# Performance work log

Measured on AMD Instinct MI355X. Metric: run time of the kernel, lower is better.

Reference implementation:

```python
import math
import jax, jax.numpy as jnp
import numpy as np

D_MODEL = 2048
NUM_EXPERTS = 64
Z_LOSS_COEF = 1e-3
AUX_LOSS_COEF = 1e-2
CAPACITY_FACTOR = 1.0
MIN_CAPACITY = 4


def setup_inputs() -> dict:
    key = jax.random.key(0)
    kx, kw = jax.random.split(key)
    x = jax.random.normal(kx, (4, 4096, D_MODEL), dtype=jnp.float32)
    W = 0.02 * jax.random.normal(kw, (NUM_EXPERTS, D_MODEL), dtype=jnp.float32)  # gate weight [E, D]
    return {"x": x, "W": W}


def reference(x, W):
    B, T, D = x.shape
    N = B * T                      # num_tokens
    E = W.shape[0]
    x_flat = x.reshape(N, D)

    logits = jnp.einsum("nd,ed->ne", x_flat, W)          # gate GEMM [N, E]
    probs = jax.nn.softmax(logits, axis=-1)

    # z-loss: mean(logsumexp(logits)^2)
    z_loss = jnp.mean(jnp.square(jax.nn.logsumexp(logits, axis=-1)))

    expert_index = jnp.argmax(logits, axis=-1)            # [N] int
    expert_prob = jnp.take_along_axis(probs, expert_index[:, None], axis=-1)[:, 0]  # [N]

    counts = jnp.bincount(expert_index, length=E)         # [E] int
    f_i = counts.astype(probs.dtype) / N                  # fraction routed per expert
    p_i = jnp.mean(probs, axis=0)                         # mean router prob per expert
    aux_loss = AUX_LOSS_COEF * E * jnp.sum(f_i * p_i) + Z_LOSS_COEF * z_loss

    capacity = max(MIN_CAPACITY, math.ceil(CAPACITY_FACTOR * N / E))  # static int
    return expert_index, expert_prob, counts, capacity, aux_loss
```

## Files before the change

### kernel.cpp

```cpp
#include <hip/hip_runtime.h>
#include <math.h>

#define D_MODEL 2048
#define NE      64
#define TB      64
#define KSEG    1024
#define KC      128
#define NCH     (KSEG / KC)
#define FB_KC   32
#define FB_NCH  (D_MODEL / FB_KC)

typedef _Float16 half8 __attribute__((ext_vector_type(8)));
typedef float    f32x4 __attribute__((ext_vector_type(4)));

#define CVT1(F, HV, LV, J) do {                                               \
    float _f = (F);                                                           \
    _Float16 _h = (_Float16)_f;                                               \
    HV[J] = _h;                                                               \
    LV[J] = (_Float16)(_f - (float)_h);                                       \
} while (0)

__global__ __launch_bounds__(256) void wcvt_kernel(
    const float* __restrict__ W, short* __restrict__ Wh, short* __restrict__ Wl)
{
    const int e = blockIdx.x, t = threadIdx.x, c = t * 8;
    const float* src = W + (size_t)e * D_MODEL + c;
    float4 v0 = *(const float4*)src;
    float4 v1 = *(const float4*)(src + 4);
    half8 hv, lv;
    CVT1(v0.x * 64.0f, hv, lv, 0); CVT1(v0.y * 64.0f, hv, lv, 1);
    CVT1(v0.z * 64.0f, hv, lv, 2); CVT1(v0.w * 64.0f, hv, lv, 3);
    CVT1(v1.x * 64.0f, hv, lv, 4); CVT1(v1.y * 64.0f, hv, lv, 5);
    CVT1(v1.z * 64.0f, hv, lv, 6); CVT1(v1.w * 64.0f, hv, lv, 7);
    *(half8*)(Wh + (size_t)e * D_MODEL + c) = hv;
    *(half8*)(Wl + (size_t)e * D_MODEL + c) = lv;
}

__global__ __launch_bounds__(512) void router_fused8(
    const float* __restrict__ x, const short* __restrict__ Whg,
    const short* __restrict__ Wlg, float* __restrict__ out,
    float* __restrict__ ws_prob, float* __restrict__ ws_z,
    int* __restrict__ ws_cnt, int Ntok)
{
    __shared__ __align__(16) char smem[131072];

    const int t  = threadIdx.x;
    const int b  = blockIdx.x;
    const int m0 = b * TB;
    const int g  = t >> 8;
    const int tg = t & 255;
    const int l  = tg & 63;
    const int wv = tg >> 6;
    const int k0 = g * KSEG;

    char* gb = smem + g * 65536;
    _Float16* Ah = (_Float16*)gb;
    _Float16* Al = (_Float16*)(gb + 16384);
    _Float16* Wh = (_Float16*)(gb + 32768);
    _Float16* Wl = (_Float16*)(gb + 49152);

    float (*sL)[NE + 1] = (float (*)[NE + 1])smem;
    float (*red8)[8]    = (float (*)[8])(smem + 16640);
    int   (*arg8)[8]    = (int (*)[8])(smem + 18688);
    float* smax         = (float*)(smem + 20736);
    float* sinv         = (float*)(smem + 20992);
    float (*spart)[NE]  = (float (*)[NE])(smem + 21248);
    int*   hist         = (int*)(smem + 23296);

    const int srow  = tg >> 4;
    const int sslt  = tg & 15;
    const int soff0 = ((sslt ^ (srow & 7)) << 3);

    float4 paA0, paA1, paA2, paA3, paA4, paA5, paA6, paA7;
    float4 paB0, paB1, paB2, paB3, paB4, paB5, paB6, paB7;
    uint4  pwh0, pwh1, pwh2, pwh3, pwl0, pwl1, pwl2, pwl3;

#define PRE_A(P0, P1, P2, P3, P4, P5, P6, P7, KB) do {                        \
    const float* _a0 = x + (size_t)(m0 +  0 + srow) * D_MODEL + (KB) + sslt * 8; \
    const float* _a1 = x + (size_t)(m0 + 16 + srow) * D_MODEL + (KB) + sslt * 8; \
    const float* _a2 = x + (size_t)(m0 + 32 + srow) * D_MODEL + (KB) + sslt * 8; \
    const float* _a3 = x + (size_t)(m0 + 48 + srow) * D_MODEL + (KB) + sslt * 8; \
    P0 = *(const float4*)_a0; P1 = *(const float4*)(_a0 + 4);                 \
    P2 = *(const float4*)_a1; P3 = *(const float4*)(_a1 + 4);                 \
    P4 = *(const float4*)_a2; P5 = *(const float4*)(_a2 + 4);                 \
    P6 = *(const float4*)_a3; P7 = *(const float4*)(_a3 + 4);                 \
} while (0)

#define PRE_W(KB) do {                                                        \
    const size_t _w0 = (size_t)( 0 + srow) * D_MODEL + (KB) + sslt * 8;       \
    const size_t _w1 = (size_t)(16 + srow) * D_MODEL + (KB) + sslt * 8;       \
    const size_t _w2 = (size_t)(32 + srow) * D_MODEL + (KB) + sslt * 8;       \
    const size_t _w3 = (size_t)(48 + srow) * D_MODEL + (KB) + sslt * 8;       \
    pwh0 = *(const uint4*)&Whg[_w0]; pwh1 = *(const uint4*)&Whg[_w1];         \
    pwh2 = *(const uint4*)&Whg[_w2]; pwh3 = *(const uint4*)&Whg[_w3];         \
    pwl0 = *(const uint4*)&Wlg[_w0]; pwl1 = *(const uint4*)&Wlg[_w1];         \
    pwl2 = *(const uint4*)&Wlg[_w2]; pwl3 = *(const uint4*)&Wlg[_w3];         \
} while (0)

#define STORE_ITEM(I, PA, PB, PWH, PWL) do {                                  \
    half8 _hv, _lv;                                                           \
    CVT1((PA).x * 8.0f, _hv, _lv, 0); CVT1((PA).y * 8.0f, _hv, _lv, 1);       \
    CVT1((PA).z * 8.0f, _hv, _lv, 2); CVT1((PA).w * 8.0f, _hv, _lv, 3);       \
    CVT1((PB).x * 8.0f, _hv, _lv, 4); CVT1((PB).y * 8.0f, _hv, _lv, 5);       \
    CVT1((PB).z * 8.0f, _hv, _lv, 6); CVT1((PB).w * 8.0f, _hv, _lv, 7);       \
    const int _off = ((I) * 16 + srow) * 128 + soff0;                         \
    *(half8*)&Ah[_off] = _hv;                                                 \
    *(half8*)&Al[_off] = _lv;                                                 \
    *(uint4*)&Wh[_off] = PWH;                                                 \
    *(uint4*)&Wl[_off] = PWL;                                                 \
} while (0)

#define STORE_SET(P0, P1, P2, P3, P4, P5, P6, P7) do {                        \
    STORE_ITEM(0, P0, P1, pwh0, pwl0);                                        \
    STORE_ITEM(1, P2, P3, pwh1, pwl1);                                        \
    STORE_ITEM(2, P4, P5, pwh2, pwl2);                                        \
    STORE_ITEM(3, P6, P7, pwh3, pwl3);                                        \
} while (0)

#define MFMA_PHASE() do {                                                     \
    const int arow = wv * 16 + (l & 15);                                      \
    const int rsw  = l & 7;                                                   \
    _Pragma("unroll")                                                         \
    for (int kq = 0; kq < 4; ++kq) {                                          \
        const int s    = kq * 4 + (l >> 4);                                   \
        const int aoff = arow * 128 + ((s ^ rsw) << 3);                       \
        half8 ah = *(const half8*)&Ah[aoff];                                  \
        half8 al = *(const half8*)&Al[aoff];                                  \
        _Pragma("unroll")                                                     \
        for (int n = 0; n < 4; ++n) {                                         \
            const int woff = (n * 16 + (l & 15)) * 128 + ((s ^ rsw) << 3);    \
            half8 wh = *(const half8*)&Wh[woff];                              \
            half8 wl = *(const half8*)&Wl[woff];                              \
            f32x4 a = (n == 0) ? acc0 : (n == 1) ? acc1 : (n == 2) ? acc2 : acc3; \
            a = __builtin_amdgcn_mfma_f32_16x16x32_f16(al, wl, a, 0, 0, 0);   \
            a = __builtin_amdgcn_mfma_f32_16x16x32_f16(al, wh, a, 0, 0, 0);   \
            a = __builtin_amdgcn_mfma_f32_16x16x32_f16(ah, wl, a, 0, 0, 0);   \
            a = __builtin_amdgcn_mfma_f32_16x16x32_f16(ah, wh, a, 0, 0, 0);   \
            if (n == 0) acc0 = a; else if (n == 1) acc1 = a;                  \
            else if (n == 2) acc2 = a; else acc3 = a;                         \
        }                                                                     \
    }                                                                         \
} while (0)

    f32x4 acc0 = {0.f,0.f,0.f,0.f}, acc1 = {0.f,0.f,0.f,0.f};
    f32x4 acc2 = {0.f,0.f,0.f,0.f}, acc3 = {0.f,0.f,0.f,0.f};

    PRE_A(paA0, paA1, paA2, paA3, paA4, paA5, paA6, paA7, k0);
    PRE_W(k0);
    PRE_A(paB0, paB1, paB2, paB3, paB4, paB5, paB6, paB7, k0 + KC);

    for (int ch = 0; ch < NCH; ch += 2) {
        __builtin_amdgcn_s_barrier();
        STORE_SET(paA0, paA1, paA2, paA3, paA4, paA5, paA6, paA7);
        asm volatile("s_waitcnt lgkmcnt(0)" ::: "memory");
        __builtin_amdgcn_s_barrier();
        if (ch + 1 < NCH) PRE_W(k0 + (ch + 1) * KC);
        if (ch + 2 < NCH)
            PRE_A(paA0, paA1, paA2, paA3, paA4, paA5, paA6, paA7, k0 + (ch + 2) * KC);
        MFMA_PHASE();
        __builtin_amdgcn_s_barrier();
        STORE_SET(paB0, paB1, paB2, paB3, paB4, paB5, paB6, paB7);
        asm volatile("s_waitcnt lgkmcnt(0)" ::: "memory");
        __builtin_amdgcn_s_barrier();
        if (ch + 2 < NCH) PRE_W(k0 + (ch + 2) * KC);
        if (ch + 3 < NCH)
            PRE_A(paB0, paB1, paB2, paB3, paB4, paB5, paB6, paB7, k0 + (ch + 3) * KC);
        MFMA_PHASE();
    }

    __syncthreads();
    const int rbase = wv * 16 + (l >> 4) * 4;
    const int col0  = l & 15;
    if (g == 1) {
        #pragma unroll
        for (int q = 0; q < 4; ++q) {
            sL[rbase + q][ 0 + col0] = acc0[q];
            sL[rbase + q][16 + col0] = acc1[q];
            sL[rbase + q][32 + col0] = acc2[q];
            sL[rbase + q][48 + col0] = acc3[q];
        }
    }
    __syncthreads();
    if (g == 0) {
        #pragma unroll
        for (int q = 0; q < 4; ++q) {
            sL[rbase + q][ 0 + col0] = (acc0[q] + sL[rbase + q][ 0 + col0]) * (1.0f / 512.0f);
            sL[rbase + q][16 + col0] = (acc1[q] + sL[rbase + q][16 + col0]) * (1.0f / 512.0f);
            sL[rbase + q][32 + col0] = (acc2[q] + sL[rbase + q][32 + col0]) * (1.0f / 512.0f);
            sL[rbase + q][48 + col0] = (acc3[q] + sL[rbase + q][48 + col0]) * (1.0f / 512.0f);
        }
    }
    if (t < NE) hist[t] = 0;
    __syncthreads();

    {
        const int m = t >> 3, qr = t & 7;
        float mx = -3.4e38f; int ag = qr * 8;
        #pragma unroll
        for (int k = 0; k < 8; ++k) {
            const int e = qr * 8 + k;
            float v = sL[m][e];
            if (v > mx) { mx = v; ag = e; }
        }
        red8[m][qr] = mx; arg8[m][qr] = ag;
    }
    __syncthreads();
    if (t < 64) {
        const int m = t;
        float mx = red8[m][0]; int ag = arg8[m][0];
        #pragma unroll
        for (int qr = 1; qr < 8; ++qr)
            if (red8[m][qr] > mx) { mx = red8[m][qr]; ag = arg8[m][qr]; }
        smax[m] = mx;
        out[m0 + m] = (float)ag;
        atomicAdd(&hist[ag], 1);
    }
    __syncthreads();
    {
        const int m = t >> 3, qr = t & 7;
        const float mx = smax[m];
        float s = 0.f;
        #pragma unroll
        for (int k = 0; k < 8; ++k) s += expf(sL[m][qr * 8 + k] - mx);
        red8[m][qr] = s;
    }
    __syncthreads();
    if (t < 64) {
        const int m = t;
        float s = 0.f;
        #pragma unroll
        for (int qr = 0; qr < 8; ++qr) s += red8[m][qr];
        float inv = 1.f / s;
        sinv[m] = inv;
        out[Ntok + m0 + m] = inv;
        float lse = smax[m] + logf(s);
        float z = lse * lse;
        #pragma unroll
        for (int off = 32; off > 0; off >>= 1) z += __shfl_down(z, off, 64);
        if (t == 0) ws_z[b] = z;
    }
    __syncthreads();
    {
        const int e = t & 63, gw = t >> 6;
        float pa = 0.f;
        #pragma unroll
        for (int k = 0; k < 8; ++k) {
            const int m = gw * 8 + k;
            pa += expf(sL[m][e] - smax[m]) * sinv[m];
        }
        spart[gw][e] = pa;
    }
    __syncthreads();
    if (t < NE) {
        float ps = 0.f;
        #pragma unroll
        for (int gw = 0; gw < 8; ++gw) ps += spart[gw][t];
        ws_prob[b * NE + t] = ps;
        ws_cnt[b * NE + t]  = hist[t];
    }
}

__global__ __launch_bounds__(256) void router_final2(
    const float* __restrict__ ws_prob, const float* __restrict__ ws_z,
    const int* __restrict__ ws_cnt, float* __restrict__ out,
    int Ntok, int nblocks)
{
    __shared__ float sp[4][NE];
    __shared__ int   sc[4][NE];
    __shared__ float sz[4];

    const int e = threadIdx.x & 63, g = threadIdx.x >> 6;
    const int per = nblocks / 4;
    const int hi  = (g == 3) ? nblocks : (g + 1) * per;

    float ps = 0.f; int c = 0;
    for (int blk = g * per; blk < hi; ++blk) {
        ps += ws_prob[blk * NE + e];
        c  += ws_cnt[blk * NE + e];
    }
    sp[g][e] = ps; sc[g][e] = c;

    float z = 0.f;
    for (int blk = (int)threadIdx.x; blk < nblocks; blk += 256) z += ws_z[blk];
    #pragma unroll
    for (int off = 32; off > 0; off >>= 1) z += __shfl_down(z, off, 64);
    if (e == 0) sz[g] = z;
    __syncthreads();

    if (threadIdx.x < 64) {
        const int ee = threadIdx.x;
        float pst = ((sp[0][ee] + sp[1][ee]) + sp[2][ee]) + sp[3][ee];
        int   ct  = ((sc[0][ee] + sc[1][ee]) + sc[2][ee]) + sc[3][ee];
        out[2 * Ntok + ee] = (float)ct;

        float fN = (float)Ntok;
        float fp = ((float)ct / fN) * (pst / fN);
        #pragma unroll
        for (int off = 32; off > 0; off >>= 1) fp += __shfl_down(fp, off, 64);
        if (ee == 0) {
            float zt = ((sz[0] + sz[1]) + sz[2]) + sz[3];
            int cap = (Ntok + NE - 1) / NE;
            if (cap < 4) cap = 4;
            float aux = 0.01f * (float)NE * fp + 1e-3f * (zt / fN);
            out[2 * Ntok + NE]     = (float)cap;
            out[2 * Ntok + NE + 1] = aux;
        }
    }
}

__global__ __launch_bounds__(256) void router_main_fb(
    const float* __restrict__ x, const float* __restrict__ W,
    float* __restrict__ out, float* __restrict__ ws_prob,
    float* __restrict__ ws_z, int* __restrict__ ws_cnt, int Ntok)
{
    __shared__ __align__(16) float sX[FB_KC][68];
    __shared__ __align__(16) float sW[FB_KC][68];
    __shared__ float sL[64][65];
    __shared__ float smax[64], sinv[64];
    __shared__ float spart[4][NE];
    __shared__ int   hist[NE];

    const int t = threadIdx.x, b = blockIdx.x, m0 = b * 64;
    const int mq = t & 15, nq = t >> 4;
    const int r1 = t >> 3, r2 = r1 + 32, c1 = (t & 7) << 2;
    const float* xp1 = x + (size_t)(m0 + r1) * D_MODEL + c1;
    const float* xp2 = x + (size_t)(m0 + r2) * D_MODEL + c1;
    const float* wp1 = W + (size_t)r1 * D_MODEL + c1;
    const float* wp2 = W + (size_t)r2 * D_MODEL + c1;
    float4 ax1 = *(const float4*)xp1, ax2 = *(const float4*)xp2;
    float4 aw1 = *(const float4*)wp1, aw2 = *(const float4*)wp2;
    float a1[4][4] = {}, a2[4][4] = {};
    for (int ch = 0; ch < FB_NCH; ++ch) {
        __syncthreads();
        sX[c1+0][r1] = ax1.x; sX[c1+1][r1] = ax1.y; sX[c1+2][r1] = ax1.z; sX[c1+3][r1] = ax1.w;
        sX[c1+0][r2] = ax2.x; sX[c1+1][r2] = ax2.y; sX[c1+2][r2] = ax2.z; sX[c1+3][r2] = ax2.w;
        sW[c1+0][r1] = aw1.x; sW[c1+1][r1] = aw1.y; sW[c1+2][r1] = aw1.z; sW[c1+3][r1] = aw1.w;
        sW[c1+0][r2] = aw2.x; sW[c1+1][r2] = aw2.y; sW[c1+2][r2] = aw2.z; sW[c1+3][r2] = aw2.w;
        __syncthreads();
        if (ch + 1 < FB_NCH) {
            xp1 += FB_KC; xp2 += FB_KC; wp1 += FB_KC; wp2 += FB_KC;
            ax1 = *(const float4*)xp1; ax2 = *(const float4*)xp2;
            aw1 = *(const float4*)wp1; aw2 = *(const float4*)wp2;
        }
        #pragma unroll
        for (int k = 0; k < FB_KC; ++k) {
            float4 xa = *(const float4*)&sX[k][mq << 2];
            float4 wb = *(const float4*)&sW[k][nq << 2];
            float (*A)[4] = (k < FB_KC / 2) ? a1 : a2;
            A[0][0] = fmaf(xa.x, wb.x, A[0][0]); A[0][1] = fmaf(xa.x, wb.y, A[0][1]);
            A[0][2] = fmaf(xa.x, wb.z, A[0][2]); A[0][3] = fmaf(xa.x, wb.w, A[0][3]);
            A[1][0] = fmaf(xa.y, wb.x, A[1][0]); A[1][1] = fmaf(xa.y, wb.y, A[1][1]);
            A[1][2] = fmaf(xa.y, wb.z, A[1][2]); A[1][3] = fmaf(xa.y, wb.w, A[1][3]);
            A[2][0] = fmaf(xa.z, wb.x, A[2][0]); A[2][1] = fmaf(xa.z, wb.y, A[2][1]);
            A[2][2] = fmaf(xa.z, wb.z, A[2][2]); A[2][3] = fmaf(xa.z, wb.w, A[2][3]);
            A[3][0] = fmaf(xa.w, wb.x, A[3][0]); A[3][1] = fmaf(xa.w, wb.y, A[3][1]);
            A[3][2] = fmaf(xa.w, wb.z, A[3][2]); A[3][3] = fmaf(xa.w, wb.w, A[3][3]);
        }
    }
    #pragma unroll
    for (int i = 0; i < 4; ++i)
        #pragma unroll
        for (int j = 0; j < 4; ++j)
            sL[(mq << 2) + i][(nq << 2) + j] = a1[i][j] + a2[i][j];
    if (t < NE) hist[t] = 0;
    __syncthreads();
    if (t < 64) {
        const int m = t;
        float mx = sL[m][0]; int arg = 0;
        for (int e = 1; e < NE; ++e) { float v = sL[m][e]; if (v > mx) { mx = v; arg = e; } }
        float s = 0.f;
        for (int e = 0; e < NE; ++e) s += expf(sL[m][e] - mx);
        float inv = 1.f / s;
        out[m0 + m] = (float)arg; out[Ntok + m0 + m] = inv;
        smax[m] = mx; sinv[m] = inv;
        atomicAdd(&hist[arg], 1);
        float lse = mx + logf(s); float z = lse * lse;
        for (int off = 32; off > 0; off >>= 1) z += __shfl_down(z, off, 64);
        if (t == 0) ws_z[b] = z;
    }
    __syncthreads();
    {
        const int e = t & 63, mg = t >> 6;
        float pa = 0.f;
        for (int m = mg * 16; m < mg * 16 + 16; ++m) pa += expf(sL[m][e] - smax[m]) * sinv[m];
        spart[mg][e] = pa;
    }
    __syncthreads();
    if (t < NE) {
        ws_prob[b * NE + t] = spart[0][t] + spart[1][t] + spart[2][t] + spart[3][t];
        ws_cnt[b * NE + t]  = hist[t];
    }
}

extern "C" void kernel_launch(void* const* d_in, const int* in_sizes, int n_in,
                              void* d_out, int out_size, void* d_ws, size_t ws_size,
                              hipStream_t stream)
{
    const float* x = (const float*)d_in[0];
    const float* W = (const float*)d_in[1];
    float* out = (float*)d_out;

    const int Ntok = in_sizes[0] / D_MODEL;
    const int nblk = Ntok / TB;

    const size_t wh_elems = (size_t)NE * D_MODEL;
    const size_t need = wh_elems * 2 * 2
                      + ((size_t)nblk * NE + nblk) * 4
                      + (size_t)nblk * NE * 4 + 1024;

    if ((Ntok % TB) == 0 && (nblk % 4) == 0 && ws_size >= need) {
        short* wsh     = (short*)d_ws;
        short* wsl     = wsh + wh_elems;
        float* ws_prob = (float*)(wsl + wh_elems);
        float* ws_z    = ws_prob + (size_t)nblk * NE;
        int*   ws_cnt  = (int*)(ws_z + nblk);

        wcvt_kernel<<<NE, 256, 0, stream>>>(W, wsh, wsl);
        router_fused8<<<nblk, 512, 0, stream>>>(x, wsh, wsl, out,
                                                ws_prob, ws_z, ws_cnt, Ntok);
        router_final2<<<1, 256, 0, stream>>>(ws_prob, ws_z, ws_cnt, out, Ntok, nblk);
    } else {
        const int nb = Ntok / 64;
        float* ws_prob = (float*)d_ws;
        float* ws_z    = ws_prob + (size_t)nb * NE;
        int*   ws_cnt  = (int*)(ws_z + nb);
        router_main_fb<<<nb, 256, 0, stream>>>(x, W, out, ws_prob, ws_z, ws_cnt, Ntok);
        router_final2<<<1, 256, 0, stream>>>(ws_prob, ws_z, ws_cnt, out, Ntok, nb);
    }
}
```

Measured before the change: 61.72 us.

## Double-buffer LDS tiles with halved K chunk to overlap stores and MFMA

Halves the K chunk from 128 to 64 and splits each group's 64KB shared region into two 32KB buffers, so the next chunk's converted A and W tiles are written to one buffer while MFMAs read the other. This drops one barrier per chunk and overlaps LDS stores with matrix math. The global load pattern also changes: each thread now loads one row with contiguous 16-element segments instead of four rows of 8 elements. In exchange there are twice as many chunks, each with less MFMA work to hide latency behind, and register-held prefetch now covers both A and W for two sets.

```diff
diff --git a/kernel.cpp b/kernel.cpp
--- a/kernel.cpp
+++ b/kernel.cpp
@@ -5,7 +5,7 @@
 #define NE      64
 #define TB      64
 #define KSEG    1024
-#define KC      128
+#define KC      64
 #define NCH     (KSEG / KC)
 #define FB_KC   32
 #define FB_NCH  (D_MODEL / FB_KC)
@@ -36,7 +36,7 @@
     *(half8*)(Wl + (size_t)e * D_MODEL + c) = lv;
 }
 
-__global__ __launch_bounds__(512) void router_fused8(
+__global__ __launch_bounds__(512) void router_fused_db(
     const float* __restrict__ x, const short* __restrict__ Whg,
     const short* __restrict__ Wlg, float* __restrict__ out,
     float* __restrict__ ws_prob, float* __restrict__ ws_z,
@@ -53,11 +53,7 @@
     const int wv = tg >> 6;
     const int k0 = g * KSEG;
 
-    char* gb = smem + g * 65536;
-    _Float16* Ah = (_Float16*)gb;
-    _Float16* Al = (_Float16*)(gb + 16384);
-    _Float16* Wh = (_Float16*)(gb + 32768);
-    _Float16* Wl = (_Float16*)(gb + 49152);
+    char* gbase = smem + g * 65536;
 
     float (*sL)[NE + 1] = (float (*)[NE + 1])smem;
     float (*red8)[8]    = (float (*)[8])(smem + 16640);
@@ -67,70 +63,64 @@
     float (*spart)[NE]  = (float (*)[NE])(smem + 21248);
     int*   hist         = (int*)(smem + 23296);
 
-    const int srow  = tg >> 4;
-    const int sslt  = tg & 15;
-    const int soff0 = ((sslt ^ (srow & 7)) << 3);
-
-    float4 paA0, paA1, paA2, paA3, paA4, paA5, paA6, paA7;
-    float4 paB0, paB1, paB2, paB3, paB4, paB5, paB6, paB7;
-    uint4  pwh0, pwh1, pwh2, pwh3, pwl0, pwl1, pwl2, pwl3;
-
-#define PRE_A(P0, P1, P2, P3, P4, P5, P6, P7, KB) do {                        \
-    const float* _a0 = x + (size_t)(m0 +  0 + srow) * D_MODEL + (KB) + sslt * 8; \
-    const float* _a1 = x + (size_t)(m0 + 16 + srow) * D_MODEL + (KB) + sslt * 8; \
-    const float* _a2 = x + (size_t)(m0 + 32 + srow) * D_MODEL + (KB) + sslt * 8; \
-    const float* _a3 = x + (size_t)(m0 + 48 + srow) * D_MODEL + (KB) + sslt * 8; \
-    P0 = *(const float4*)_a0; P1 = *(const float4*)(_a0 + 4);                 \
-    P2 = *(const float4*)_a1; P3 = *(const float4*)(_a1 + 4);                 \
-    P4 = *(const float4*)_a2; P5 = *(const float4*)(_a2 + 4);                 \
-    P6 = *(const float4*)_a3; P7 = *(const float4*)(_a3 + 4);                 \
+    const int srow = tg >> 2;
+    const int sc   = tg & 3;
+    const int ssw  = srow & 7;
+    const int sof0 = (srow << 6) + (((sc * 2 + 0) ^ ssw) << 3);
+    const int sof1 = (srow << 6) + (((sc * 2 + 1) ^ ssw) << 3);
+
+    float4 aA0, aA1, aA2, aA3;
+    float4 aB0, aB1, aB2, aB3;
+    uint4  whA0, whA1, wlA0, wlA1;
+    uint4  whB0, whB1, wlB0, wlB1;
+
+#define PRE_SET(A0, A1, A2, A3, WH0, WH1, WL0, WL1, KB) do {                  \
+    const float* _ap = x + (size_t)(m0 + srow) * D_MODEL + (KB) + sc * 16;    \
+    A0 = *(const float4*)_ap;       A1 = *(const float4*)(_ap + 4);           \
+    A2 = *(const float4*)(_ap + 8); A3 = *(const float4*)(_ap + 12);          \
+    const size_t _wr = (size_t)srow * D_MODEL + (KB) + sc * 16;               \
+    WH0 = *(const uint4*)&Whg[_wr]; WH1 = *(const uint4*)&Whg[_wr + 8];       \
+    WL0 = *(const uint4*)&Wlg[_wr]; WL1 = *(const uint4*)&Wlg[_wr + 8];       \
 } while (0)
 
-#define PRE_W(KB) do {                                                        \
-    const size_t _w0 = (size_t)( 0 + srow) * D_MODEL + (KB) + sslt * 8;       \
-    const size_t _w1 = (size_t)(16 + srow) * D_MODEL + (KB) + sslt * 8;       \
-    const size_t _w2 = (size_t)(32 + srow) * D_MODEL + (KB) + sslt * 8;       \
-    const size_t _w3 = (size_t)(48 + srow) * D_MODEL + (KB) + sslt * 8;       \
-    pwh0 = *(const uint4*)&Whg[_w0]; pwh1 = *(const uint4*)&Whg[_w1];         \
-    pwh2 = *(const uint4*)&Whg[_w2]; pwh3 = *(const uint4*)&Whg[_w3];         \
-    pwl0 = *(const uint4*)&Wlg[_w0]; pwl1 = *(const uint4*)&Wlg[_w1];         \
-    pwl2 = *(const uint4*)&Wlg[_w2]; pwl3 = *(const uint4*)&Wlg[_w3];         \
+#define STORE_SET(A0, A1, A2, A3, WH0, WH1, WL0, WL1, BB) do {                \
+    _Float16* _Ah = (_Float16*)(gbase + (BB) * 32768);                        \
+    _Float16* _Al = (_Float16*)(gbase + (BB) * 32768 + 8192);                 \
+    _Float16* _Wh = (_Float16*)(gbase + (BB) * 32768 + 16384);                \
+    _Float16* _Wl = (_Float16*)(gbase + (BB) * 32768 + 24576);                \
+    half8 _h0, _l0, _h1, _l1;                                                 \
+    CVT1((A0).x * 8.0f, _h0, _l0, 0); CVT1((A0).y * 8.0f, _h0, _l0, 1);       \
+    CVT1((A0).z * 8.0f, _h0, _l0, 2); CVT1((A0).w * 8.0f, _h0, _l0, 3);       \
+    CVT1((A1).x * 8.0f, _h0, _l0, 4); CVT1((A1).y * 8.0f, _h0, _l0, 5);       \
+    CVT1((A1).z * 8.0f, _h0, _l0, 6); CVT1((A1).w * 8.0f, _h0, _l0, 7);       \
+    CVT1((A2).x * 8.0f, _h1, _l1, 0); CVT1((A2).y * 8.0f, _h1, _l1, 1);       \
+    CVT1((A2).z * 8.0f, _h1, _l1, 2); CVT1((A2).w * 8.0f, _h1, _l1, 3);       \
+    CVT1((A3).x * 8.0f, _h1, _l1, 4); CVT1((A3).y * 8.0f, _h1, _l1, 5);       \
+    CVT1((A3).z * 8.0f, _h1, _l1, 6); CVT1((A3).w * 8.0f, _h1, _l1, 7);       \
+    *(half8*)&_Ah[sof0] = _h0;  *(half8*)&_Ah[sof1] = _h1;                    \
+    *(half8*)&_Al[sof0] = _l0;  *(half8*)&_Al[sof1] = _l1;                    \
+    *(uint4*)&_Wh[sof0] = WH0;  *(uint4*)&_Wh[sof1] = WH1;                    \
+    *(uint4*)&_Wl[sof0] = WL0;  *(uint4*)&_Wl[sof1] = WL1;                    \
 } while (0)
 
-#define STORE_ITEM(I, PA, PB, PWH, PWL) do {                                  \
-    half8 _hv, _lv;                                                           \
-    CVT1((PA).x * 8.0f, _hv, _lv, 0); CVT1((PA).y * 8.0f, _hv, _lv, 1);       \
-    CVT1((PA).z * 8.0f, _hv, _lv, 2); CVT1((PA).w * 8.0f, _hv, _lv, 3);       \
-    CVT1((PB).x * 8.0f, _hv, _lv, 4); CVT1((PB).y * 8.0f, _hv, _lv, 5);       \
-    CVT1((PB).z * 8.0f, _hv, _lv, 6); CVT1((PB).w * 8.0f, _hv, _lv, 7);       \
-    const int _off = ((I) * 16 + srow) * 128 + soff0;                         \
-    *(half8*)&Ah[_off] = _hv;                                                 \
-    *(half8*)&Al[_off] = _lv;                                                 \
-    *(uint4*)&Wh[_off] = PWH;                                                 \
-    *(uint4*)&Wl[_off] = PWL;                                                 \
-} while (0)
-
-#define STORE_SET(P0, P1, P2, P3, P4, P5, P6, P7) do {                        \
-    STORE_ITEM(0, P0, P1, pwh0, pwl0);                                        \
-    STORE_ITEM(1, P2, P3, pwh1, pwl1);                                        \
-    STORE_ITEM(2, P4, P5, pwh2, pwl2);                                        \
-    STORE_ITEM(3, P6, P7, pwh3, pwl3);                                        \
-} while (0)
-
-#define MFMA_PHASE() do {                                                     \
+#define MFMA_PHASE(BB) do {                                                   \
+    const _Float16* _Ah = (const _Float16*)(gbase + (BB) * 32768);            \
+    const _Float16* _Al = (const _Float16*)(gbase + (BB) * 32768 + 8192);     \
+    const _Float16* _Wh = (const _Float16*)(gbase + (BB) * 32768 + 16384);    \
+    const _Float16* _Wl = (const _Float16*)(gbase + (BB) * 32768 + 24576);    \
     const int arow = wv * 16 + (l & 15);                                      \
     const int rsw  = l & 7;                                                   \
     _Pragma("unroll")                                                         \
-    for (int kq = 0; kq < 4; ++kq) {                                          \
+    for (int kq = 0; kq < 2; ++kq) {                                          \
         const int s    = kq * 4 + (l >> 4);                                   \
-        const int aoff = arow * 128 + ((s ^ rsw) << 3);                       \
-        half8 ah = *(const half8*)&Ah[aoff];                                  \
-        half8 al = *(const half8*)&Al[aoff];                                  \
+        const int aoff = arow * 64 + ((s ^ rsw) << 3);                        \
+        half8 ah = *(const half8*)&_Ah[aoff];                                 \
+        half8 al = *(const half8*)&_Al[aoff];                                 \
         _Pragma("unroll")                                                     \
         for (int n = 0; n < 4; ++n) {                                         \
-            const int woff = (n * 16 + (l & 15)) * 128 + ((s ^ rsw) << 3);    \
-            half8 wh = *(const half8*)&Wh[woff];                              \
-            half8 wl = *(const half8*)&Wl[woff];                              \
+            const int woff = (n * 16 + (l & 15)) * 64 + ((s ^ rsw) << 3);     \
+            half8 wh = *(const half8*)&_Wh[woff];                             \
+            half8 wl = *(const half8*)&_Wl[woff];                             \
             f32x4 a = (n == 0) ? acc0 : (n == 1) ? acc1 : (n == 2) ? acc2 : acc3; \
             a = __builtin_amdgcn_mfma_f32_16x16x32_f16(al, wl, a, 0, 0, 0);   \
             a = __builtin_amdgcn_mfma_f32_16x16x32_f16(al, wh, a, 0, 0, 0);   \
@@ -145,27 +135,27 @@
     f32x4 acc0 = {0.f,0.f,0.f,0.f}, acc1 = {0.f,0.f,0.f,0.f};
     f32x4 acc2 = {0.f,0.f,0.f,0.f}, acc3 = {0.f,0.f,0.f,0.f};
 
-    PRE_A(paA0, paA1, paA2, paA3, paA4, paA5, paA6, paA7, k0);
-    PRE_W(k0);
-    PRE_A(paB0, paB1, paB2, paB3, paB4, paB5, paB6, paB7, k0 + KC);
+    PRE_SET(aA0, aA1, aA2, aA3, whA0, whA1, wlA0, wlA1, k0);
+    PRE_SET(aB0, aB1, aB2, aB3, whB0, whB1, wlB0, wlB1, k0 + KC);
+    STORE_SET(aA0, aA1, aA2, aA3, whA0, whA1, wlA0, wlA1, 0);
+    asm volatile("s_waitcnt lgkmcnt(0)" ::: "memory");
+    __builtin_amdgcn_s_barrier();
 
     for (int ch = 0; ch < NCH; ch += 2) {
-        __builtin_amdgcn_s_barrier();
-        STORE_SET(paA0, paA1, paA2, paA3, paA4, paA5, paA6, paA7);
+        if (ch + 2 < NCH)
+            PRE_SET(aA0, aA1, aA2, aA3, whA0, whA1, wlA0, wlA1, k0 + (ch + 2) * KC);
+        if (ch + 1 < NCH)
+            STORE_SET(aB0, aB1, aB2, aB3, whB0, whB1, wlB0, wlB1, 1);
+        MFMA_PHASE(0);
         asm volatile("s_waitcnt lgkmcnt(0)" ::: "memory");
         __builtin_amdgcn_s_barrier();
-        if (ch + 1 < NCH) PRE_W(k0 + (ch + 1) * KC);
+        if (ch + 3 < NCH)
+            PRE_SET(aB0, aB1, aB2, aB3, whB0, whB1, wlB0, wlB1, k0 + (ch + 3) * KC);
         if (ch + 2 < NCH)
-            PRE_A(paA0, paA1, paA2, paA3, paA4, paA5, paA6, paA7, k0 + (ch + 2) * KC);
-        MFMA_PHASE();
-        __builtin_amdgcn_s_barrier();
-        STORE_SET(paB0, paB1, paB2, paB3, paB4, paB5, paB6, paB7);
+            STORE_SET(aA0, aA1, aA2, aA3, whA0, whA1, wlA0, wlA1, 0);
+        MFMA_PHASE(1);
         asm volatile("s_waitcnt lgkmcnt(0)" ::: "memory");
         __builtin_amdgcn_s_barrier();
-        if (ch + 2 < NCH) PRE_W(k0 + (ch + 2) * KC);
-        if (ch + 3 < NCH)
-            PRE_A(paB0, paB1, paB2, paB3, paB4, paB5, paB6, paB7, k0 + (ch + 3) * KC);
-        MFMA_PHASE();
     }
 
     __syncthreads();
@@ -416,8 +406,8 @@
         int*   ws_cnt  = (int*)(ws_z + nblk);
 
         wcvt_kernel<<<NE, 256, 0, stream>>>(W, wsh, wsl);
-        router_fused8<<<nblk, 512, 0, stream>>>(x, wsh, wsl, out,
-                                                ws_prob, ws_z, ws_cnt, Ntok);
+        router_fused_db<<<nblk, 512, 0, stream>>>(x, wsh, wsl, out,
+                                                  ws_prob, ws_z, ws_cnt, Ntok);
         router_final2<<<1, 256, 0, stream>>>(ws_prob, ws_z, ws_cnt, out, Ntok, nblk);
     } else {
         const int nb = Ntok / 64;
```

Measured after the change: 59.61 us. -3.4%, faster.
